# Kernel tuning notes

Measured on AMD Instinct MI355X. Metric: run time of the kernel, lower is better.

## Reference

```python
import jax, jax.numpy as jnp
import numpy as np

N, D, DFF, E, K = 2048, 1024, 4096, 8, 2  # tokens, d_model, d_ff, num_expert, top_k


def setup_inputs() -> dict:
    key = jax.random.key(0)
    ks = jax.random.split(key, 5)
    s = 0.02  # init scale
    return {
        "moe_inp": jax.random.normal(ks[0], (N, D), jnp.float32),
        "Wg": jax.random.normal(ks[1], (D, E), jnp.float32) * s,   # gate linear
        "bg": jnp.zeros((E,), jnp.float32),
        "W1": jax.random.normal(ks[2], (E, D, DFF), jnp.float32) * s,  # htoh4 per expert
        "b1": jnp.zeros((E, DFF), jnp.float32),
        "W2": jax.random.normal(ks[3], (E, DFF, D), jnp.float32) * s,  # h4toh per expert
        "b2": jnp.zeros((E, D), jnp.float32),
    }


def reference(moe_inp, Wg, bg, W1, b1, W2, b2):
    # --- NaiveGate: top-k experts per token, softmax over selected logits ---
    logits = moe_inp @ Wg + bg                      # [N, E]
    top_val, top_idx = jax.lax.top_k(logits, K)     # [N, K]
    score = jax.nn.softmax(top_val, axis=-1)        # [N, K]

    # Dense combine weights c[n, e] = sum_j score[n, j] * 1{top_idx[n, j] == e}.
    # This is the mathematically exact equivalent of scatter -> grouped expert
    # GEMM -> gather -> score-weighted combine in fmoe.
    comb = jnp.einsum(
        "nke,nk->ne", jax.nn.one_hot(top_idx, E, dtype=moe_inp.dtype), score
    )                                               # [N, E]

    # --- per-expert FFN: relu(x W1 + b1) W2 + b2, masked-combined by comb ---
    h = jax.nn.relu(jnp.einsum("nd,edh->enh", moe_inp, W1) + b1[:, None, :])  # [E, N, DFF]
    out = jnp.einsum("enh,ehd,ne->nd", h, W2, comb) + comb @ b2               # [N, D]
    return out
```

## Files before the change

kernel.cpp:

```cpp
#include <hip/hip_runtime.h>
#include <hip/hip_bf16.h>
#include <cstdint>
#include <cstddef>

#define NTOKS  2048
#define DMODEL 1024
#define DFFN   4096
#define NEXP   8

typedef __attribute__((ext_vector_type(8))) short short8;
typedef __attribute__((ext_vector_type(4))) float f32x4;
typedef __attribute__((ext_vector_type(4))) unsigned short u16x4;
typedef __attribute__((ext_vector_type(8))) unsigned short u16x8;

static constexpr size_t alignup(size_t x) { return (x + 255) & ~(size_t)255; }
static constexpr size_t OFF_XB   = 0;
static constexpr size_t OFF_CNT  = alignup(OFF_XB + (size_t)(NTOKS + 1) * DMODEL * 2);
static constexpr size_t OFF_OFFS = OFF_CNT + 256;
static constexpr size_t OFF_TOKE = OFF_OFFS + 256;
static constexpr size_t OFF_TOKT = OFF_TOKE + (size_t)NTOKS * 2 * 4;
static constexpr size_t OFF_TOKS = OFF_TOKT + (size_t)NTOKS * 2 * 4;
static constexpr size_t OFF_CAP  = alignup(OFF_TOKS + (size_t)NTOKS * 2 * 4);
static constexpr size_t OFF_H    = alignup(OFF_CAP + (size_t)NEXP * NTOKS * 4);
static constexpr size_t OFF_Y    = alignup(OFF_H + (size_t)(NTOKS * 2 + 128) * DFFN * 2);
static constexpr size_t OFF_WB   = alignup(OFF_Y + (size_t)NTOKS * 2 * DMODEL * 4);

__device__ inline unsigned short f2bf(float f) {
  __hip_bfloat16 h = __float2bfloat16(f);
  return __builtin_bit_cast(unsigned short, h);
}

__device__ inline void gload16(const void* g, void* l) {
  __builtin_amdgcn_global_load_lds((const __attribute__((address_space(1))) unsigned int*)g,
                                   (__attribute__((address_space(3))) unsigned int*)l, 16, 0, 0);
}

__global__ __launch_bounds__(256) void k_convert(const float* __restrict__ x,
                                                 unsigned short* __restrict__ xb,
                                                 int* __restrict__ cnt) {
  if (blockIdx.x == 0 && threadIdx.x < NEXP) cnt[threadIdx.x] = 0;
  size_t base = ((size_t)blockIdx.x * 256 + threadIdx.x) * 8;
  const size_t total = (size_t)(NTOKS + 1) * DMODEL;
  if (base >= total) return;
  u16x8 o;
  if (base < (size_t)NTOKS * DMODEL) {
    f32x4 a = *(const f32x4*)(x + base);
    f32x4 b = *(const f32x4*)(x + base + 4);
#pragma unroll
    for (int j = 0; j < 4; ++j) { o[j] = f2bf(a[j]); o[4 + j] = f2bf(b[j]); }
  } else {
#pragma unroll
    for (int j = 0; j < 8; ++j) o[j] = 0;
  }
  *(u16x8*)(xb + base) = o;
}

template <int R, int C>
__global__ __launch_bounds__(256) void k_transconv(const float* __restrict__ W,
                                                   unsigned short* __restrict__ WT) {
  __shared__ unsigned short T[64][66];
  const int e = blockIdx.z;
  const int c0 = blockIdx.x * 64, r0 = blockIdx.y * 64;
  const float* Wp = W + (size_t)e * R * C;
  unsigned short* Tp = WT + (size_t)e * R * C;
  const int tid = threadIdx.x;
  const int rr = tid >> 4, cc = (tid & 15) << 2;
#pragma unroll
  for (int i = 0; i < 4; ++i) {
    int r = rr + (i << 4);
    f32x4 v = *(const f32x4*)(Wp + (size_t)(r0 + r) * C + c0 + cc);
    T[r][cc]     = f2bf(v[0]);
    T[r][cc + 1] = f2bf(v[1]);
    T[r][cc + 2] = f2bf(v[2]);
    T[r][cc + 3] = f2bf(v[3]);
  }
  __syncthreads();
  const int c = tid >> 2, kc = (tid & 3) << 4;
  u16x8 o0, o1;
#pragma unroll
  for (int i = 0; i < 8; ++i) { o0[i] = T[kc + i][c]; o1[i] = T[kc + 8 + i][c]; }
  unsigned short* dst = Tp + (size_t)(c0 + c) * R + r0 + kc;
  *(u16x8*)(dst) = o0;
  *(u16x8*)(dst + 8) = o1;
}

__global__ __launch_bounds__(256) void k_gate(const float* __restrict__ x,
                                              const float* __restrict__ Wg,
                                              const float* __restrict__ bg,
                                              int* __restrict__ cnt,
                                              int* __restrict__ tok_e,
                                              int* __restrict__ tok_t,
                                              float* __restrict__ tok_s,
                                              int* __restrict__ cap) {
  const int w = threadIdx.x >> 6, lane = threadIdx.x & 63;
  const int n = blockIdx.x * 4 + w;
  float acc[8];
#pragma unroll
  for (int e = 0; e < 8; ++e) acc[e] = 0.f;
  const float* xr = x + (size_t)n * DMODEL;
#pragma unroll 4
  for (int it = 0; it < DMODEL / 64; ++it) {
    int d = it * 64 + lane;
    float xv = xr[d];
    f32x4 w0 = *(const f32x4*)(Wg + d * 8);
    f32x4 w1 = *(const f32x4*)(Wg + d * 8 + 4);
#pragma unroll
    for (int j = 0; j < 4; ++j) { acc[j] += xv * w0[j]; acc[4 + j] += xv * w1[j]; }
  }
#pragma unroll
  for (int e = 0; e < 8; ++e)
#pragma unroll
    for (int off = 32; off; off >>= 1) acc[e] += __shfl_xor(acc[e], off, 64);
  if (lane == 0) {
    float l[8];
#pragma unroll
    for (int e = 0; e < 8; ++e) l[e] = acc[e] + bg[e];
    int i0 = 0; float v0 = l[0];
#pragma unroll
    for (int e = 1; e < 8; ++e) if (l[e] > v0) { v0 = l[e]; i0 = e; }
    int i1 = (i0 == 0) ? 1 : 0; float v1 = l[i1];
#pragma unroll
    for (int e = 0; e < 8; ++e) if (e != i0 && l[e] > v1) { v1 = l[e]; i1 = e; }
    float t = expf(v1 - v0);
    float inv = 1.f / (1.f + t);
    float s0 = inv, s1 = t * inv;
    int t0 = atomicAdd(&cnt[i0], 1);
    int t1 = atomicAdd(&cnt[i1], 1);
    cap[i0 * NTOKS + t0] = n;
    cap[i1 * NTOKS + t1] = n;
    tok_e[2 * n] = i0; tok_e[2 * n + 1] = i1;
    tok_t[2 * n] = t0; tok_t[2 * n + 1] = t1;
    tok_s[2 * n] = s0; tok_s[2 * n + 1] = s1;
  }
}

__global__ void k_scan(const int* __restrict__ cnt, int* __restrict__ offs) {
  if (threadIdx.x == 0) {
    int s = 0;
#pragma unroll
    for (int e = 0; e < NEXP; ++e) { offs[e] = s; s += cnt[e]; }
  }
}

template <int KTOT, int NTOT, int BN, bool FIRST>
__global__ __launch_bounds__(256) void k_gemm(const unsigned short* __restrict__ Asrc,
                                              const unsigned short* __restrict__ Bsrc,
                                              const float* __restrict__ bias,
                                              const int* __restrict__ cnt,
                                              const int* __restrict__ offs,
                                              const int* __restrict__ cap,
                                              unsigned short* __restrict__ hout,
                                              float* __restrict__ yout) {
  const int e = blockIdx.y >> 4, tile = blockIdx.y & 15;
  const int c = cnt[e];
  const int t0 = tile * 128;
  if (t0 >= c) return;
  const int base = offs[e] + t0;
  const int n0 = blockIdx.x * BN;

  const int tid = threadIdx.x, w = tid >> 6, lane = tid & 63;
  const int l15 = lane & 15, lq = lane >> 4;
  constexpr int MR = 4;
  constexpr int NR = BN / 32;
  constexpr int NT = KTOT / 64;
  constexpr int BROUNDS = BN / 32;
  const int wr = w >> 1, wc = w & 1;

  __shared__ unsigned short As[2][128 * 64];
  __shared__ unsigned short Bs[2][BN * 64];

  const int rl = tid >> 3;
  const int sw = ((tid & 7) ^ (rl & 7)) << 3;
  const unsigned short* aptr[4];
#pragma unroll
  for (int r = 0; r < 4; ++r) {
    int row = r * 32 + rl;
    size_t gr;
    if constexpr (FIRST) gr = (size_t)((t0 + row < c) ? cap[e * NTOKS + t0 + row] : NTOKS);
    else                 gr = (size_t)(base + row);
    aptr[r] = Asrc + gr * (size_t)KTOT + sw;
  }
  const unsigned short* Be = Bsrc + (size_t)e * ((size_t)KTOT * NTOT);
  const unsigned short* bptr[BROUNDS];
#pragma unroll
  for (int r = 0; r < BROUNDS; ++r)
    bptr[r] = Be + (size_t)(n0 + r * 32 + rl) * KTOT + sw;

  auto stageA = [&](int k0, int b) {
#pragma unroll
    for (int r = 0; r < 4; ++r)
      gload16(aptr[r] + k0, &As[b][(r * 32 + (w << 3)) << 6]);
  };
  auto stageB = [&](int k0, int b) {
#pragma unroll
    for (int r = 0; r < BROUNDS; ++r)
      gload16(bptr[r] + k0, &Bs[b][(r * 32 + (w << 3)) << 6]);
  };

  f32x4 acc[MR][NR] = {};

  stageA(0, 0);
  stageB(0, 0);
  __syncthreads();

  int buf = 0;
  for (int t = 0; t < NT; ++t) {
    const int nxt = buf ^ 1;
    if (t + 1 < NT) { stageA((t + 1) << 6, nxt); stageB((t + 1) << 6, nxt); }

    short8 a0[MR], a1[MR], b0[NR], b1[NR];
    const int sw0 = (lq ^ (l15 & 7)) << 3;
#pragma unroll
    for (int m = 0; m < MR; ++m) {
      const unsigned short* ab = &As[buf][(wr * 64 + m * 16 + l15) << 6];
      a0[m] = *(const short8*)&ab[sw0];
      a1[m] = *(const short8*)&ab[sw0 ^ 32];
    }
#pragma unroll
    for (int nn = 0; nn < NR; ++nn) {
      const unsigned short* bb = &Bs[buf][(wc * (BN / 2) + nn * 16 + l15) << 6];
      b0[nn] = *(const short8*)&bb[sw0];
      b1[nn] = *(const short8*)&bb[sw0 ^ 32];
    }
#pragma unroll
    for (int m = 0; m < MR; ++m)
#pragma unroll
      for (int nn = 0; nn < NR; ++nn) {
        acc[m][nn] = __builtin_amdgcn_mfma_f32_16x16x32_bf16(a0[m], b0[nn], acc[m][nn], 0, 0, 0);
        acc[m][nn] = __builtin_amdgcn_mfma_f32_16x16x32_bf16(a1[m], b1[nn], acc[m][nn], 0, 0, 0);
      }

    __syncthreads();
    buf = nxt;
  }

  if constexpr (FIRST) {
    const float* be = bias + (size_t)e * NTOT;
#pragma unroll
    for (int m = 0; m < MR; ++m) {
#pragma unroll
      for (int q = 0; q < 4; ++q) {
        int row = wr * 64 + m * 16 + lq * 4 + q;
        if (t0 + row < c) {
          unsigned short* hr = hout + (size_t)(base + row) * NTOT;
#pragma unroll
          for (int nn = 0; nn < NR; ++nn) {
            int col = n0 + wc * (BN / 2) + nn * 16 + l15;
            float v = acc[m][nn][q] + be[col];
            v = v > 0.f ? v : 0.f;
            hr[col] = f2bf(v);
          }
        }
      }
    }
  } else {
#pragma unroll
    for (int m = 0; m < MR; ++m) {
#pragma unroll
      for (int q = 0; q < 4; ++q) {
        int row = wr * 64 + m * 16 + lq * 4 + q;
        if (t0 + row < c) {
          float* yr = yout + (size_t)(base + row) * NTOT;
#pragma unroll
          for (int nn = 0; nn < NR; ++nn) {
            int col = n0 + wc * (BN / 2) + nn * 16 + l15;
            yr[col] = acc[m][nn][q];
          }
        }
      }
    }
  }
}

__global__ __launch_bounds__(256) void k_combine(const float* __restrict__ y,
                                                 const float* __restrict__ b2,
                                                 const int* __restrict__ tok_e,
                                                 const int* __restrict__ tok_t,
                                                 const float* __restrict__ tok_s,
                                                 const int* __restrict__ offs,
                                                 float* __restrict__ out) {
  const int n = blockIdx.x, t = threadIdx.x;
  const int e0 = tok_e[2 * n], e1 = tok_e[2 * n + 1];
  const int s0i = offs[e0] + tok_t[2 * n];
  const int s1i = offs[e1] + tok_t[2 * n + 1];
  const float sc0 = tok_s[2 * n], sc1 = tok_s[2 * n + 1];
  f32x4 v0 = *(const f32x4*)(y + (size_t)s0i * DMODEL + t * 4);
  f32x4 v1 = *(const f32x4*)(y + (size_t)s1i * DMODEL + t * 4);
  f32x4 c0 = *(const f32x4*)(b2 + (size_t)e0 * DMODEL + t * 4);
  f32x4 c1 = *(const f32x4*)(b2 + (size_t)e1 * DMODEL + t * 4);
  f32x4 r = sc0 * (v0 + c0) + sc1 * (v1 + c1);
  *(f32x4*)(out + (size_t)n * DMODEL + t * 4) = r;
}

extern "C" void kernel_launch(void* const* d_in, const int* in_sizes, int n_in,
                              void* d_out, int out_size, void* d_ws, size_t ws_size,
                              hipStream_t stream) {
  const float* x  = (const float*)d_in[0];
  const float* Wg = (const float*)d_in[1];
  const float* bg = (const float*)d_in[2];
  const float* W1 = (const float*)d_in[3];
  const float* b1 = (const float*)d_in[4];
  const float* W2 = (const float*)d_in[5];
  const float* b2 = (const float*)d_in[6];
  float* out = (float*)d_out;

  char* ws = (char*)d_ws;
  unsigned short* xb = (unsigned short*)(ws + OFF_XB);
  int*   cnt   = (int*)(ws + OFF_CNT);
  int*   offs  = (int*)(ws + OFF_OFFS);
  int*   tok_e = (int*)(ws + OFF_TOKE);
  int*   tok_t = (int*)(ws + OFF_TOKT);
  float* tok_s = (float*)(ws + OFF_TOKS);
  int*   cap   = (int*)(ws + OFF_CAP);
  unsigned short* h  = (unsigned short*)(ws + OFF_H);
  float* y = (float*)(ws + OFF_Y);
  unsigned short* wb = (unsigned short*)(ws + OFF_WB);

  const int convBlocks = (int)(((size_t)(NTOKS + 1) * DMODEL / 8 + 255) / 256);
  k_convert<<<convBlocks, 256, 0, stream>>>(x, xb, cnt);
  k_gate<<<NTOKS / 4, 256, 0, stream>>>(x, Wg, bg, cnt, tok_e, tok_t, tok_s, cap);
  k_scan<<<1, 64, 0, stream>>>(cnt, offs);

  k_transconv<DMODEL, DFFN><<<dim3(DFFN / 64, DMODEL / 64, NEXP), 256, 0, stream>>>(W1, wb);
  k_gemm<DMODEL, DFFN, 128, true><<<dim3(DFFN / 128, NEXP * 16), 256, 0, stream>>>(
      xb, wb, b1, cnt, offs, cap, h, nullptr);

  k_transconv<DFFN, DMODEL><<<dim3(DMODEL / 64, DFFN / 64, NEXP), 256, 0, stream>>>(W2, wb);
  k_gemm<DFFN, DMODEL, 64, false><<<dim3(DMODEL / 64, NEXP * 16), 256, 0, stream>>>(
      h, wb, nullptr, cnt, offs, cap, nullptr, y);

  k_combine<<<NTOKS, 256, 0, stream>>>(y, b2, tok_e, tok_t, tok_s, offs, out);
}
```

Baseline: 287.8 us.

## Prefetch two K-tiles ahead with explicit waitcnt and remap blocks per XCD

The grouped GEMM kernel now issues loads for both the first and second K-tiles before entering the loop. Each iteration waits on vmcnt only for the current tile, uses raw s_barriers instead of __syncthreads, and raises wave priority around the MFMA block, so global loads overlap compute more deeply. Block indices are also remapped so that consecutive tiles of the same expert row-block land on the same XCD, which is meant to improve L2 reuse of A and B. The hand-set vmcnt values depend on the exact number of loads issued per stage, so the code is fragile if BN or the load count changes.

Result: slower. 341.1 us (+18.5%).

```diff
diff --git a/kernel.cpp b/kernel.cpp
--- a/kernel.cpp
+++ b/kernel.cpp
@@ -151,12 +151,17 @@
                                               const int* __restrict__ cap,
                                               unsigned short* __restrict__ hout,
                                               float* __restrict__ yout) {
-  const int e = blockIdx.y >> 4, tile = blockIdx.y & 15;
+  constexpr int NBLK = NTOT / BN;
+  const int f = blockIdx.y * NBLK + blockIdx.x;
+  const int xcd = f & 7, q = f >> 3;
+  const int j = q % NBLK, gq = q / NBLK;
+  const int g = gq * 8 + xcd;
+  const int e = g >> 4, tile = g & 15;
   const int c = cnt[e];
   const int t0 = tile * 128;
   if (t0 >= c) return;
   const int base = offs[e] + t0;
-  const int n0 = blockIdx.x * BN;
+  const int n0 = j * BN;
 
   const int tid = threadIdx.x, w = tid >> 6, lane = tid & 63;
   const int l15 = lane & 15, lq = lane >> 4;
@@ -201,27 +206,41 @@
 
   stageA(0, 0);
   stageB(0, 0);
-  __syncthreads();
-
-  int buf = 0;
+  stageA(64, 1);
+  stageB(64, 1);
+
   for (int t = 0; t < NT; ++t) {
-    const int nxt = buf ^ 1;
-    if (t + 1 < NT) { stageA((t + 1) << 6, nxt); stageB((t + 1) << 6, nxt); }
+    const int cur = t & 1;
+    if (t < NT - 1) {
+      if constexpr (BN == 128) asm volatile("s_waitcnt vmcnt(8)" ::: "memory");
+      else                     asm volatile("s_waitcnt vmcnt(6)" ::: "memory");
+    } else {
+      asm volatile("s_waitcnt vmcnt(0)" ::: "memory");
+    }
+    __builtin_amdgcn_sched_barrier(0);
+    __builtin_amdgcn_s_barrier();
 
     short8 a0[MR], a1[MR], b0[NR], b1[NR];
     const int sw0 = (lq ^ (l15 & 7)) << 3;
 #pragma unroll
     for (int m = 0; m < MR; ++m) {
-      const unsigned short* ab = &As[buf][(wr * 64 + m * 16 + l15) << 6];
+      const unsigned short* ab = &As[cur][(wr * 64 + m * 16 + l15) << 6];
       a0[m] = *(const short8*)&ab[sw0];
       a1[m] = *(const short8*)&ab[sw0 ^ 32];
     }
 #pragma unroll
     for (int nn = 0; nn < NR; ++nn) {
-      const unsigned short* bb = &Bs[buf][(wc * (BN / 2) + nn * 16 + l15) << 6];
+      const unsigned short* bb = &Bs[cur][(wc * (BN / 2) + nn * 16 + l15) << 6];
       b0[nn] = *(const short8*)&bb[sw0];
       b1[nn] = *(const short8*)&bb[sw0 ^ 32];
     }
+    asm volatile("s_waitcnt lgkmcnt(0)" ::: "memory");
+    __builtin_amdgcn_sched_barrier(0);
+    __builtin_amdgcn_s_barrier();
+
+    if (t + 2 < NT) { stageA((t + 2) << 6, cur); stageB((t + 2) << 6, cur); }
+
+    __builtin_amdgcn_s_setprio(1);
 #pragma unroll
     for (int m = 0; m < MR; ++m)
 #pragma unroll
@@ -229,9 +248,7 @@
         acc[m][nn] = __builtin_amdgcn_mfma_f32_16x16x32_bf16(a0[m], b0[nn], acc[m][nn], 0, 0, 0);
         acc[m][nn] = __builtin_amdgcn_mfma_f32_16x16x32_bf16(a1[m], b1[nn], acc[m][nn], 0, 0, 0);
       }
-
-    __syncthreads();
-    buf = nxt;
+    __builtin_amdgcn_s_setprio(0);
   }
 
   if constexpr (FIRST) {
@@ -239,14 +256,14 @@
 #pragma unroll
     for (int m = 0; m < MR; ++m) {
 #pragma unroll
-      for (int q = 0; q < 4; ++q) {
-        int row = wr * 64 + m * 16 + lq * 4 + q;
+      for (int q2 = 0; q2 < 4; ++q2) {
+        int row = wr * 64 + m * 16 + lq * 4 + q2;
         if (t0 + row < c) {
           unsigned short* hr = hout + (size_t)(base + row) * NTOT;
 #pragma unroll
           for (int nn = 0; nn < NR; ++nn) {
             int col = n0 + wc * (BN / 2) + nn * 16 + l15;
-            float v = acc[m][nn][q] + be[col];
+            float v = acc[m][nn][q2] + be[col];
             v = v > 0.f ? v : 0.f;
             hr[col] = f2bf(v);
           }
@@ -257,14 +274,14 @@
 #pragma unroll
     for (int m = 0; m < MR; ++m) {
 #pragma unroll
-      for (int q = 0; q < 4; ++q) {
-        int row = wr * 64 + m * 16 + lq * 4 + q;
+      for (int q2 = 0; q2 < 4; ++q2) {
+        int row = wr * 64 + m * 16 + lq * 4 + q2;
         if (t0 + row < c) {
           float* yr = yout + (size_t)(base + row) * NTOT;
 #pragma unroll
           for (int nn = 0; nn < NR; ++nn) {
             int col = n0 + wc * (BN / 2) + nn * 16 + l15;
-            yr[col] = acc[m][nn][q];
+            yr[col] = acc[m][nn][q2];
           }
         }
       }
```

## Split-K the second expert GEMM and remap blocks across XCDs

Applied to the files above, without the earlier changes.

The second grouped GEMM (K=4096) is split into two K halves along grid z. Each half writes a separate fp32 partial buffer, and the combine kernel sums the two partials. Both GEMMs also remap the flat block index so that consecutive blocks spread across the 8 XCDs, grouping the token tiles of an expert for L2 reuse of weights. This raises parallelism for the small-N second GEMM at the cost of doubling the y buffer traffic and adding extra reads in combine.

Result: slower. 348.8 us (+21.2%).

```diff
diff --git a/kernel.cpp b/kernel.cpp
--- a/kernel.cpp
+++ b/kernel.cpp
@@ -23,7 +23,7 @@
 static constexpr size_t OFF_CAP  = alignup(OFF_TOKS + (size_t)NTOKS * 2 * 4);
 static constexpr size_t OFF_H    = alignup(OFF_CAP + (size_t)NEXP * NTOKS * 4);
 static constexpr size_t OFF_Y    = alignup(OFF_H + (size_t)(NTOKS * 2 + 128) * DFFN * 2);
-static constexpr size_t OFF_WB   = alignup(OFF_Y + (size_t)NTOKS * 2 * DMODEL * 4);
+static constexpr size_t OFF_WB   = alignup(OFF_Y + (size_t)2 * NTOKS * 2 * DMODEL * 4);
 
 __device__ inline unsigned short f2bf(float f) {
   __hip_bfloat16 h = __float2bfloat16(f);
@@ -142,7 +142,7 @@
   }
 }
 
-template <int KTOT, int NTOT, int BN, bool FIRST>
+template <int KTOT, int NTOT, int BN, bool FIRST, int KSPLIT>
 __global__ __launch_bounds__(256) void k_gemm(const unsigned short* __restrict__ Asrc,
                                               const unsigned short* __restrict__ Bsrc,
                                               const float* __restrict__ bias,
@@ -151,18 +151,25 @@
                                               const int* __restrict__ cap,
                                               unsigned short* __restrict__ hout,
                                               float* __restrict__ yout) {
-  const int e = blockIdx.y >> 4, tile = blockIdx.y & 15;
+  constexpr int NBLK = NTOT / BN;
+  constexpr int KCH = KTOT / KSPLIT;
+  constexpr int NT = KCH / 64;
+  const int f = blockIdx.y * NBLK + blockIdx.x;
+  const int xcd = f & 7, q = f >> 3;
+  const int j = q % NBLK, gq = q / NBLK;
+  const int g = gq * 8 + xcd;
+  const int e = g >> 4, tile = g & 15;
   const int c = cnt[e];
   const int t0 = tile * 128;
   if (t0 >= c) return;
   const int base = offs[e] + t0;
-  const int n0 = blockIdx.x * BN;
+  const int n0 = j * BN;
+  const int kb = blockIdx.z * KCH;
 
   const int tid = threadIdx.x, w = tid >> 6, lane = tid & 63;
   const int l15 = lane & 15, lq = lane >> 4;
   constexpr int MR = 4;
   constexpr int NR = BN / 32;
-  constexpr int NT = KTOT / 64;
   constexpr int BROUNDS = BN / 32;
   const int wr = w >> 1, wc = w & 1;
 
@@ -178,13 +185,13 @@
     size_t gr;
     if constexpr (FIRST) gr = (size_t)((t0 + row < c) ? cap[e * NTOKS + t0 + row] : NTOKS);
     else                 gr = (size_t)(base + row);
-    aptr[r] = Asrc + gr * (size_t)KTOT + sw;
+    aptr[r] = Asrc + gr * (size_t)KTOT + kb + sw;
   }
   const unsigned short* Be = Bsrc + (size_t)e * ((size_t)KTOT * NTOT);
   const unsigned short* bptr[BROUNDS];
 #pragma unroll
   for (int r = 0; r < BROUNDS; ++r)
-    bptr[r] = Be + (size_t)(n0 + r * 32 + rl) * KTOT + sw;
+    bptr[r] = Be + (size_t)(n0 + r * 32 + rl) * KTOT + kb + sw;
 
   auto stageA = [&](int k0, int b) {
 #pragma unroll
@@ -239,14 +246,14 @@
 #pragma unroll
     for (int m = 0; m < MR; ++m) {
 #pragma unroll
-      for (int q = 0; q < 4; ++q) {
-        int row = wr * 64 + m * 16 + lq * 4 + q;
+      for (int q2 = 0; q2 < 4; ++q2) {
+        int row = wr * 64 + m * 16 + lq * 4 + q2;
         if (t0 + row < c) {
           unsigned short* hr = hout + (size_t)(base + row) * NTOT;
 #pragma unroll
           for (int nn = 0; nn < NR; ++nn) {
             int col = n0 + wc * (BN / 2) + nn * 16 + l15;
-            float v = acc[m][nn][q] + be[col];
+            float v = acc[m][nn][q2] + be[col];
             v = v > 0.f ? v : 0.f;
             hr[col] = f2bf(v);
           }
@@ -254,17 +261,18 @@
       }
     }
   } else {
+    float* yz = yout + (size_t)blockIdx.z * NTOKS * 2 * DMODEL;
 #pragma unroll
     for (int m = 0; m < MR; ++m) {
 #pragma unroll
-      for (int q = 0; q < 4; ++q) {
-        int row = wr * 64 + m * 16 + lq * 4 + q;
+      for (int q2 = 0; q2 < 4; ++q2) {
+        int row = wr * 64 + m * 16 + lq * 4 + q2;
         if (t0 + row < c) {
-          float* yr = yout + (size_t)(base + row) * NTOT;
+          float* yr = yz + (size_t)(base + row) * NTOT;
 #pragma unroll
           for (int nn = 0; nn < NR; ++nn) {
             int col = n0 + wc * (BN / 2) + nn * 16 + l15;
-            yr[col] = acc[m][nn][q];
+            yr[col] = acc[m][nn][q2];
           }
         }
       }
@@ -280,15 +288,18 @@
                                                  const int* __restrict__ offs,
                                                  float* __restrict__ out) {
   const int n = blockIdx.x, t = threadIdx.x;
+  const float* y1 = y + (size_t)NTOKS * 2 * DMODEL;
   const int e0 = tok_e[2 * n], e1 = tok_e[2 * n + 1];
   const int s0i = offs[e0] + tok_t[2 * n];
   const int s1i = offs[e1] + tok_t[2 * n + 1];
   const float sc0 = tok_s[2 * n], sc1 = tok_s[2 * n + 1];
   f32x4 v0 = *(const f32x4*)(y + (size_t)s0i * DMODEL + t * 4);
+  f32x4 u0 = *(const f32x4*)(y1 + (size_t)s0i * DMODEL + t * 4);
   f32x4 v1 = *(const f32x4*)(y + (size_t)s1i * DMODEL + t * 4);
+  f32x4 u1 = *(const f32x4*)(y1 + (size_t)s1i * DMODEL + t * 4);
   f32x4 c0 = *(const f32x4*)(b2 + (size_t)e0 * DMODEL + t * 4);
   f32x4 c1 = *(const f32x4*)(b2 + (size_t)e1 * DMODEL + t * 4);
-  f32x4 r = sc0 * (v0 + c0) + sc1 * (v1 + c1);
+  f32x4 r = sc0 * ((v0 + u0) + c0) + sc1 * ((v1 + u1) + c1);
   *(f32x4*)(out + (size_t)n * DMODEL + t * 4) = r;
 }
 
@@ -322,11 +333,11 @@
   k_scan<<<1, 64, 0, stream>>>(cnt, offs);
 
   k_transconv<DMODEL, DFFN><<<dim3(DFFN / 64, DMODEL / 64, NEXP), 256, 0, stream>>>(W1, wb);
-  k_gemm<DMODEL, DFFN, 128, true><<<dim3(DFFN / 128, NEXP * 16), 256, 0, stream>>>(
+  k_gemm<DMODEL, DFFN, 128, true, 1><<<dim3(DFFN / 128, NEXP * 16, 1), 256, 0, stream>>>(
       xb, wb, b1, cnt, offs, cap, h, nullptr);
 
   k_transconv<DFFN, DMODEL><<<dim3(DMODEL / 64, DFFN / 64, NEXP), 256, 0, stream>>>(W2, wb);
-  k_gemm<DFFN, DMODEL, 64, false><<<dim3(DMODEL / 64, NEXP * 16), 256, 0, stream>>>(
+  k_gemm<DFFN, DMODEL, 64, false, 2><<<dim3(DMODEL / 64, NEXP * 16, 2), 256, 0, stream>>>(
       h, wb, nullptr, cnt, offs, cap, nullptr, y);
 
   k_combine<<<NTOKS, 256, 0, stream>>>(y, b2, tok_e, tok_t, tok_s, offs, out);
```
